# Kernel tuning notes

Measured on AMD Instinct MI355X. Metric: run time of the kernel, lower is better.

The kernel has to match this reference:

```python
import jax, jax.numpy as jnp
import numpy as np

K = 64
M = 256
V = 5000

def setup_inputs() -> dict:
    key = jax.random.key(0)
    ks = jax.random.split(key, 8)
    feat_x = jax.random.normal(ks[0], (1, V, M), dtype=jnp.float32)
    feat_y = jax.random.normal(ks[1], (1, V, M), dtype=jnp.float32)
    evals_x = jnp.sort(jax.random.uniform(ks[2], (1, K), dtype=jnp.float32))
    evals_y = jnp.sort(jax.random.uniform(ks[3], (1, K), dtype=jnp.float32))
    evecs_trans_x = jax.random.normal(ks[4], (1, K, V), dtype=jnp.float32) / np.sqrt(V)
    evecs_trans_y = jax.random.normal(ks[5], (1, K, V), dtype=jnp.float32) / np.sqrt(V)
    eye = jnp.eye(K, dtype=jnp.float32)
    sqrtMk_x = (eye + 0.05 * jax.random.normal(ks[6], (K, K), dtype=jnp.float32))[None]
    sqrtMk_y = (eye + 0.05 * jax.random.normal(ks[7], (K, K), dtype=jnp.float32))[None]
    return {"feat_x": feat_x, "feat_y": feat_y, "evals_x": evals_x, "evals_y": evals_y,
            "evecs_trans_x": evecs_trans_x, "evecs_trans_y": evecs_trans_y,
            "sqrtMk_x": sqrtMk_x, "sqrtMk_y": sqrtMk_y}

LMBDA = 0.001

def _fmap(fx, fy, ex, ey, tx, ty, sx, sy):
    # squeeze batch dim of 1 (as in torch .squeeze())
    fx, fy = fx[0], fy[0]            # [V, m]
    ex, ey = ex[0], ey[0]            # [k]
    tx, ty = tx[0], ty[0]            # [k, V]
    sx, sy = sx[0], sy[0]            # [k, k]
    A = tx @ fx                      # [k, m] spectral coeffs of feat_x
    B = sy @ (ty @ fy)               # adapt_feature=True: premultiply by sqrtMk_y
    k, m = A.shape
    vec_B = B.T.reshape(m * k, 1)
    At_Ik = jnp.kron(A.T, sy)        # [m*k, k*k] (adapt_feature -> Ik = sqrtMk_y)
    first = At_Ik.T @ At_Ik          # [k^2, k^2]
    # adapt_mask=True branch
    inv_sx = jnp.linalg.inv(sx)
    lx = jnp.diag(ex)
    ly = jnp.diag(ey)
    lx_Ik = jnp.kron(lx @ inv_sx, sy)
    Ik_ly = jnp.kron(inv_sx, sy @ ly)
    Delta = lx_Ik - Ik_ly
    second = Delta.T @ Delta
    rhs = At_Ik.T @ vec_B
    op = first + LMBDA * second
    C = jnp.linalg.solve(op, rhs)
    return C.reshape(k, k).T[None]   # [1, k, k]

def reference(feat_x, feat_y, evals_x, evals_y, evecs_trans_x, evecs_trans_y, sqrtMk_x, sqrtMk_y):
    # bidirectional=False -> only Cxy (Cyx is None in the torch module)
    return _fmap(feat_x, feat_y, evals_x, evals_y, evecs_trans_x, evecs_trans_y, sqrtMk_x, sqrtMk_y)
```

## Files before the change

### kernel.cpp

```cpp
#include <hip/hip_runtime.h>

#define LMBDA 0.001f
#define NS_SY 4
#define NS_G  5
#define NS_SX 5
#define OUTER 3
#define LDP 68

#define WS_A    0
#define WS_FY   16384
#define WS_G1   32768
#define WS_T1   36864
#define WS_R2   40960
#define WS_R4   45056
#define WS_GINV 49152
#define WS_C    53248
#define WS_FYAT 57344
#define WS_FLAGS 61440

#define FMA4(ar, xs, b) { ar[0]=fmaf((xs),(b).x,ar[0]); ar[1]=fmaf((xs),(b).y,ar[1]); \
                          ar[2]=fmaf((xs),(b).z,ar[2]); ar[3]=fmaf((xs),(b).w,ar[3]); }

template<int SA, int SB>
__device__ __forceinline__ void mm64(const float* __restrict__ A,
                                     const float* __restrict__ B,
                                     int ti, int tj, float a[4][4]) {
    #pragma unroll 4
    for (int k = 0; k < 64; k += 4) {
        float4 av0 = *(const float4*)&A[(4 * ti + 0) * SA + k];
        float4 av1 = *(const float4*)&A[(4 * ti + 1) * SA + k];
        float4 av2 = *(const float4*)&A[(4 * ti + 2) * SA + k];
        float4 av3 = *(const float4*)&A[(4 * ti + 3) * SA + k];
        float4 b0 = *(const float4*)&B[(k + 0) * SB + 4 * tj];
        float4 b1 = *(const float4*)&B[(k + 1) * SB + 4 * tj];
        float4 b2 = *(const float4*)&B[(k + 2) * SB + 4 * tj];
        float4 b3 = *(const float4*)&B[(k + 3) * SB + 4 * tj];
        FMA4(a[0], av0.x, b0); FMA4(a[0], av0.y, b1); FMA4(a[0], av0.z, b2); FMA4(a[0], av0.w, b3);
        FMA4(a[1], av1.x, b0); FMA4(a[1], av1.y, b1); FMA4(a[1], av1.z, b2); FMA4(a[1], av1.w, b3);
        FMA4(a[2], av2.x, b0); FMA4(a[2], av2.y, b1); FMA4(a[2], av2.z, b2); FMA4(a[2], av2.w, b3);
        FMA4(a[3], av3.x, b0); FMA4(a[3], av3.y, b1); FMA4(a[3], av3.z, b2); FMA4(a[3], av3.w, b3);
    }
}

__device__ __forceinline__ void ns_invert(float* sM, float* sX, float* sY,
                                          int iters, int ti, int tj,
                                          int tid, float alpha)
{
    for (int idx = tid; idx < 4096; idx += 256) {
        int i = idx >> 6, j = idx & 63;
        sX[i * LDP + j] = (i == j) ? alpha : 0.f;
    }
    __syncthreads();
    for (int it = 0; it < iters; ++it) {
        float y[4][4];
        #pragma unroll
        for (int r = 0; r < 4; ++r)
            #pragma unroll
            for (int c = 0; c < 4; ++c) y[r][c] = 0.f;
        mm64<LDP, LDP>(sM, sX, ti, tj, y);
        #pragma unroll
        for (int r = 0; r < 4; ++r) {
            float4 v = {y[r][0], y[r][1], y[r][2], y[r][3]};
            *(float4*)&sY[(4 * ti + r) * 64 + 4 * tj] = v;
        }
        __syncthreads();
        float z[4][4];
        #pragma unroll
        for (int r = 0; r < 4; ++r)
            #pragma unroll
            for (int c = 0; c < 4; ++c) z[r][c] = 0.f;
        mm64<LDP, 64>(sX, sY, ti, tj, z);
        __syncthreads();
        #pragma unroll
        for (int r = 0; r < 4; ++r) {
            float4 xv = *(const float4*)&sX[(4 * ti + r) * LDP + 4 * tj];
            xv.x = 2.f * xv.x - z[r][0];
            xv.y = 2.f * xv.y - z[r][1];
            xv.z = 2.f * xv.z - z[r][2];
            xv.w = 2.f * xv.w - z[r][3];
            *(float4*)&sX[(4 * ti + r) * LDP + 4 * tj] = xv;
        }
        __syncthreads();
    }
}

__device__ __forceinline__ void wait_ge(int* flag, int target, int tid) {
    if (tid == 0) {
        while (__hip_atomic_load(flag, __ATOMIC_ACQUIRE, __HIP_MEMORY_SCOPE_AGENT) < target)
            __builtin_amdgcn_s_sleep(2);
    }
    __syncthreads();
    __threadfence();
}

__device__ __forceinline__ void signal_one(int* flag, int tid) {
    __syncthreads();
    __threadfence();
    if (tid == 0)
        (void)__hip_atomic_fetch_add(flag, 1, __ATOMIC_RELEASE, __HIP_MEMORY_SCOPE_AGENT);
}

__global__ __launch_bounds__(256, 1) void fused_fmnet(
    const float* __restrict__ fx, const float* __restrict__ fy,
    const float* __restrict__ ex, const float* __restrict__ ey,
    const float* __restrict__ tx, const float* __restrict__ ty,
    const float* __restrict__ sx, const float* __restrict__ sy,
    float* __restrict__ ws, float* __restrict__ out)
{
    extern __shared__ __align__(16) float lds[];
    int* flags = (int*)(ws + WS_FLAGS);
    const int tid = threadIdx.x;
    const int ti = tid >> 4, tj = tid & 15;
    const int bid = blockIdx.x;

    if (bid < 216) {
        float* sT = lds;
        float* sF = lds + 4352;
        const int gx = bid & 7, gy = bid >> 3;
        const int mat = gx >> 2;
        const int m0 = (gx & 3) << 6;
        const float* __restrict__ T = mat ? ty : tx;
        const float* __restrict__ F = mat ? fy : fx;
        float* __restrict__ Out = ws + (mat ? WS_FY : WS_A);

        float acc[4][4];
        #pragma unroll
        for (int r = 0; r < 4; ++r)
            #pragma unroll
            for (int c = 0; c < 4; ++c) acc[r][c] = 0.f;

        for (int sc = gy; sc * 64 < 5000; sc += 27) {
            const int v0 = sc << 6;
            int vlen = 5000 - v0; if (vlen > 64) vlen = 64;
            #pragma unroll
            for (int w = 0; w < 4; ++w) {
                const int fidx = tid + (w << 8);
                const int row = fidx >> 4, q = fidx & 15;
                const int vv = q << 2;
                if (vv < vlen) {
                    float4 val = *(const float4*)(T + (size_t)row * 5000 + v0 + vv);
                    sT[(vv + 0) * LDP + row] = val.x;
                    sT[(vv + 1) * LDP + row] = val.y;
                    sT[(vv + 2) * LDP + row] = val.z;
                    sT[(vv + 3) * LDP + row] = val.w;
                }
                if (row < vlen) {
                    *(float4*)&sF[row * LDP + (q << 2)] =
                        *(const float4*)(F + (size_t)(v0 + row) * 256 + m0 + (q << 2));
                }
            }
            __syncthreads();
            for (int v = 0; v < vlen; ++v) {
                float4 av = *(const float4*)&sT[v * LDP + 4 * ti];
                float4 bv = *(const float4*)&sF[v * LDP + 4 * tj];
                FMA4(acc[0], av.x, bv); FMA4(acc[1], av.y, bv);
                FMA4(acc[2], av.z, bv); FMA4(acc[3], av.w, bv);
            }
            __syncthreads();
        }
        #pragma unroll
        for (int r = 0; r < 4; ++r)
            #pragma unroll
            for (int c = 0; c < 4; ++c)
                atomicAdd(&Out[(4 * ti + r) * 256 + m0 + 4 * tj + c], acc[r][c]);
        __syncthreads();
        __threadfence();
        if (tid == 0) {
            (void)__hip_atomic_fetch_add(&flags[gx], 1, __ATOMIC_RELEASE, __HIP_MEMORY_SCOPE_AGENT);
            (void)__hip_atomic_fetch_add(&flags[10], 1, __ATOMIC_RELEASE, __HIP_MEMORY_SCOPE_AGENT);
        }
    } else if (bid < 220) {
        const int ch = bid - 216;
        wait_ge(&flags[ch], 27, tid);
        float* sA = lds;
        for (int idx = tid; idx < 1024; idx += 256) {
            int i = idx >> 4, m4 = (idx & 15) << 2;
            *(float4*)&sA[i * LDP + m4] =
                *(const float4*)&ws[WS_A + i * 256 + (ch << 6) + m4];
        }
        __syncthreads();
        float a[4][4];
        #pragma unroll
        for (int r = 0; r < 4; ++r)
            #pragma unroll
            for (int c = 0; c < 4; ++c) a[r][c] = 0.f;
        for (int m = 0; m < 64; m += 4) {
            float4 av[4], bv[4];
            #pragma unroll
            for (int r = 0; r < 4; ++r) av[r] = *(const float4*)&sA[(4 * ti + r) * LDP + m];
            #pragma unroll
            for (int c = 0; c < 4; ++c) bv[c] = *(const float4*)&sA[(4 * tj + c) * LDP + m];
            #pragma unroll
            for (int r = 0; r < 4; ++r)
                #pragma unroll
                for (int c = 0; c < 4; ++c)
                    a[r][c] += av[r].x * bv[c].x + av[r].y * bv[c].y
                             + av[r].z * bv[c].z + av[r].w * bv[c].w;
        }
        #pragma unroll
        for (int r = 0; r < 4; ++r)
            #pragma unroll
            for (int c = 0; c < 4; ++c)
                atomicAdd(&ws[WS_G1 + (4 * ti + r) * 64 + 4 * tj + c], a[r][c]);
        __syncthreads();
        __threadfence();
        if (tid == 0)
            (void)__hip_atomic_fetch_add(&flags[8], 1, __ATOMIC_RELEASE, __HIP_MEMORY_SCOPE_AGENT);
    } else if (bid == 220) {
        float* sSy = lds;
        float* sXx = lds + 4352;
        float* sYy = lds + 8704;
        float* sH  = lds + 12800;
        float* sV  = lds + 16896;
        for (int idx = tid; idx < 1024; idx += 256) {
            int i = idx >> 4, j4 = (idx & 15) << 2;
            *(float4*)&sSy[i * LDP + j4] = *(const float4*)&sy[i * 64 + j4];
        }
        if (tid < 64) sV[tid] = ey[tid];
        __syncthreads();
        {
            float h[4][4];
            #pragma unroll
            for (int r = 0; r < 4; ++r)
                #pragma unroll
                for (int c = 0; c < 4; ++c) h[r][c] = 0.f;
            for (int k = 0; k < 64; ++k) {
                float4 av = *(const float4*)&sSy[k * LDP + 4 * ti];
                float4 bv = *(const float4*)&sSy[k * LDP + 4 * tj];
                FMA4(h[0], av.x, bv); FMA4(h[1], av.y, bv);
                FMA4(h[2], av.z, bv); FMA4(h[3], av.w, bv);
            }
            #pragma unroll
            for (int r = 0; r < 4; ++r) {
                float4 v = {h[r][0], h[r][1], h[r][2], h[r][3]};
                *(float4*)&sH[(4 * ti + r) * 64 + 4 * tj] = v;
            }
        }
        __syncthreads();
        ns_invert(sSy, sXx, sYy, NS_SY, ti, tj, tid, 1.0f);
        {
            float h[4][4];
            #pragma unroll
            for (int r = 0; r < 4; ++r)
                #pragma unroll
                for (int c = 0; c < 4; ++c) h[r][c] = 0.f;
            for (int m = 0; m < 64; m += 4) {
                float4 av[4], bv[4];
                #pragma unroll
                for (int r = 0; r < 4; ++r) av[r] = *(const float4*)&sXx[(4 * ti + r) * LDP + m];
                #pragma unroll
                for (int c = 0; c < 4; ++c) bv[c] = *(const float4*)&sXx[(4 * tj + c) * LDP + m];
                #pragma unroll
                for (int r = 0; r < 4; ++r)
                    #pragma unroll
                    for (int c = 0; c < 4; ++c)
                        h[r][c] += av[r].x * bv[c].x + av[r].y * bv[c].y
                                 + av[r].z * bv[c].z + av[r].w * bv[c].w;
            }
            __syncthreads();
            #pragma unroll
            for (int r = 0; r < 4; ++r) {
                float4 v = {h[r][0], h[r][1], h[r][2], h[r][3]};
                *(float4*)&sSy[(4 * ti + r) * LDP + 4 * tj] = v;
            }
        }
        __syncthreads();
        {
            float a[4][4];
            #pragma unroll
            for (int r = 0; r < 4; ++r)
                #pragma unroll
                for (int c = 0; c < 4; ++c) a[r][c] = 0.f;
            #pragma unroll 4
            for (int k = 0; k < 64; k += 4) {
                float4 av[4];
                #pragma unroll
                for (int r = 0; r < 4; ++r) av[r] = *(const float4*)&sSy[(4 * ti + r) * LDP + k];
                #pragma unroll
                for (int q = 0; q < 4; ++q) {
                    float e = sV[k + q];
                    float4 bv = *(const float4*)&sH[(k + q) * 64 + 4 * tj];
                    bv.x *= e; bv.y *= e; bv.z *= e; bv.w *= e;
                    float xq[4] = {av[0].x, av[1].x, av[2].x, av[3].x};
                    if (q == 1) { xq[0]=av[0].y; xq[1]=av[1].y; xq[2]=av[2].y; xq[3]=av[3].y; }
                    if (q == 2) { xq[0]=av[0].z; xq[1]=av[1].z; xq[2]=av[2].z; xq[3]=av[3].z; }
                    if (q == 3) { xq[0]=av[0].w; xq[1]=av[1].w; xq[2]=av[2].w; xq[3]=av[3].w; }
                    #pragma unroll
                    for (int r = 0; r < 4; ++r) FMA4(a[r], xq[r], bv);
                }
            }
            #pragma unroll
            for (int r = 0; r < 4; ++r) {
                float4 v = {a[r][0], a[r][1], a[r][2], a[r][3]};
                *(float4*)&ws[WS_C + (4 * ti + r) * 64 + 4 * tj] = v;
            }
        }
        signal_one(&flags[9], tid);
    } else if (bid == 221) {
        float* sM = lds;
        float* sX = lds + 4352;
        float* sY = lds + 8704;
        float* sV = lds + 12800;
        for (int idx = tid; idx < 1024; idx += 256) {
            int i = idx >> 4, j4 = (idx & 15) << 2;
            *(float4*)&sM[i * LDP + j4] = *(const float4*)&sx[i * 64 + j4];
        }
        if (tid < 64) sV[tid] = ex[tid];
        __syncthreads();
        ns_invert(sM, sX, sY, NS_SX, ti, tj, tid, 1.0f);
        float aR2[4][4], aR4[4][4], aT1[4][4];
        #pragma unroll
        for (int r = 0; r < 4; ++r)
            #pragma unroll
            for (int c = 0; c < 4; ++c) { aR2[r][c] = 0.f; aR4[r][c] = 0.f; aT1[r][c] = 0.f; }
        for (int k = 0; k < 64; ++k) {
            float e = sV[k], e2 = e * e;
            float4 av = *(const float4*)&sX[k * LDP + 4 * ti];
            float4 bv = *(const float4*)&sX[k * LDP + 4 * tj];
            float avv[4] = {av.x, av.y, av.z, av.w};
            #pragma unroll
            for (int r = 0; r < 4; ++r) {
                FMA4(aR4[r], avv[r], bv);
                float ea = e * avv[r];
                FMA4(aR2[r], ea, bv);
                float e2a = e2 * avv[r];
                FMA4(aT1[r], e2a, bv);
            }
        }
        #pragma unroll
        for (int r = 0; r < 4; ++r) {
            int o = (4 * ti + r) * 64 + 4 * tj;
            float4 v2 = {aR2[r][0], aR2[r][1], aR2[r][2], aR2[r][3]};
            float4 v4 = {aR4[r][0], aR4[r][1], aR4[r][2], aR4[r][3]};
            float4 v1 = {aT1[r][0], aT1[r][1], aT1[r][2], aT1[r][3]};
            *(float4*)&ws[WS_R2 + o] = v2;
            *(float4*)&ws[WS_R4 + o] = v4;
            *(float4*)&ws[WS_T1 + o] = v1;
        }
        signal_one(&flags[9], tid);
    } else if (bid == 222) {
        wait_ge(&flags[8], 4, tid);
        float* sG = lds;
        float* sX = lds + 4352;
        float* sY = lds + 8704;
        float* sV = lds + 12800;
        for (int idx = tid; idx < 1024; idx += 256) {
            int i = idx >> 4, j4 = (idx & 15) << 2;
            *(float4*)&sG[i * LDP + j4] = *(const float4*)&ws[WS_G1 + i * 64 + j4];
        }
        __syncthreads();
        if (tid < 64) {
            float s = 0.f;
            for (int j4 = 0; j4 < 64; j4 += 4) {
                float4 v = *(const float4*)&sG[tid * LDP + j4];
                s += v.x * v.x + v.y * v.y + v.z * v.z + v.w * v.w;
            }
            sV[tid] = s;
            sV[64 + tid] = sG[tid * LDP + tid];
        }
        __syncthreads();
        float f2 = 0.f, tr = 0.f;
        for (int i = 0; i < 64; ++i) { f2 += sV[i]; tr += sV[64 + i]; }
        ns_invert(sG, sX, sY, NS_G, ti, tj, tid, tr / f2);
        for (int idx = tid; idx < 1024; idx += 256) {
            int i = idx >> 4, j4 = (idx & 15) << 2;
            *(float4*)&ws[WS_GINV + i * 64 + j4] = *(const float4*)&sX[i * LDP + j4];
        }
        signal_one(&flags[9], tid);
    } else if (bid == 223) {
        wait_ge(&flags[10], 216, tid);
        float* sFy = lds;
        float* sAx = lds + 4352;
        float a[4][4];
        #pragma unroll
        for (int r = 0; r < 4; ++r)
            #pragma unroll
            for (int c = 0; c < 4; ++c) a[r][c] = 0.f;
        for (int ch = 0; ch < 4; ++ch) {
            for (int idx = tid; idx < 1024; idx += 256) {
                int i = idx >> 4, m4 = (idx & 15) << 2;
                *(float4*)&sFy[i * LDP + m4] = *(const float4*)&ws[WS_FY + i * 256 + (ch << 6) + m4];
                *(float4*)&sAx[i * LDP + m4] = *(const float4*)&ws[WS_A  + i * 256 + (ch << 6) + m4];
            }
            __syncthreads();
            for (int m = 0; m < 64; m += 4) {
                float4 av[4], bv[4];
                #pragma unroll
                for (int r = 0; r < 4; ++r) av[r] = *(const float4*)&sFy[(4 * ti + r) * LDP + m];
                #pragma unroll
                for (int c = 0; c < 4; ++c) bv[c] = *(const float4*)&sAx[(4 * tj + c) * LDP + m];
                #pragma unroll
                for (int r = 0; r < 4; ++r)
                    #pragma unroll
                    for (int c = 0; c < 4; ++c)
                        a[r][c] += av[r].x * bv[c].x + av[r].y * bv[c].y
                                 + av[r].z * bv[c].z + av[r].w * bv[c].w;
            }
            __syncthreads();
        }
        #pragma unroll
        for (int r = 0; r < 4; ++r) {
            float4 v = {a[r][0], a[r][1], a[r][2], a[r][3]};
            *(float4*)&ws[WS_FYAT + (4 * ti + r) * 64 + 4 * tj] = v;
        }
        signal_one(&flags[9], tid);
    } else {
        wait_ge(&flags[9], 4, tid);
        float* cM1   = lds;
        float* cR2   = lds + 4096;
        float* cR4   = lds + 8192;
        float* cGinv = lds + 12288;
        float* sE    = lds + 16384;
        float* sX    = lds + 20480;
        float* cC    = lds + 24832;
        float* sW    = lds + 29184;

        for (int idx = tid; idx < 1024; idx += 256) {
            int i = idx >> 4, j4 = (idx & 15) << 2;
            int o = i * 64 + j4;
            float4 g = *(const float4*)&ws[WS_G1 + o];
            float4 t = *(const float4*)&ws[WS_T1 + o];
            float4 m = {fmaf(LMBDA, t.x, g.x), fmaf(LMBDA, t.y, g.y),
                        fmaf(LMBDA, t.z, g.z), fmaf(LMBDA, t.w, g.w)};
            *(float4*)&cM1[o]   = m;
            *(float4*)&cR2[o]   = *(const float4*)&ws[WS_R2 + o];
            *(float4*)&cR4[o]   = *(const float4*)&ws[WS_R4 + o];
            *(float4*)&cGinv[o] = *(const float4*)&ws[WS_GINV + o];
            *(float4*)&cC[i * LDP + j4] = *(const float4*)&ws[WS_C + o];
        }
        float4 eyv = *(const float4*)&ey[4 * ti];
        float eyr[4] = {eyv.x, eyv.y, eyv.z, eyv.w};
        float leyr[4];
        #pragma unroll
        for (int r = 0; r < 4; ++r) leyr[r] = LMBDA * eyr[r];

        float fyr[4][4], xreg[4][4];
        #pragma unroll
        for (int r = 0; r < 4; ++r) {
            float4 v = *(const float4*)&ws[WS_FYAT + (4 * ti + r) * 64 + 4 * tj];
            fyr[r][0] = v.x; fyr[r][1] = v.y; fyr[r][2] = v.z; fyr[r][3] = v.w;
            float4 z = {0.f, 0.f, 0.f, 0.f};
            *(float4*)&sX[(4 * ti + r) * LDP + 4 * tj] = z;
            #pragma unroll
            for (int c = 0; c < 4; ++c) xreg[r][c] = 0.f;
        }
        __syncthreads();

        float E1[4][4];
        for (int it = 0; it < OUTER; ++it) {
            {
                float Sm[4][4], S2[4][4], S4[4][4];
                #pragma unroll
                for (int r = 0; r < 4; ++r)
                    #pragma unroll
                    for (int c = 0; c < 4; ++c) { Sm[r][c] = 0.f; S2[r][c] = 0.f; S4[r][c] = 0.f; }
                #pragma unroll 2
                for (int k = 0; k < 64; k += 4) {
                    float4 av[4];
                    #pragma unroll
                    for (int r = 0; r < 4; ++r)
                        av[r] = *(const float4*)&sX[(4 * ti + r) * LDP + k];
                    #pragma unroll
                    for (int q = 0; q < 4; ++q) {
                        float4 mv = *(const float4*)&cM1[(k + q) * 64 + 4 * tj];
                        float4 qv = *(const float4*)&cR2[(k + q) * 64 + 4 * tj];
                        float4 rv = *(const float4*)&cR4[(k + q) * 64 + 4 * tj];
                        float xq[4] = {av[0].x, av[1].x, av[2].x, av[3].x};
                        if (q == 1) { xq[0]=av[0].y; xq[1]=av[1].y; xq[2]=av[2].y; xq[3]=av[3].y; }
                        if (q == 2) { xq[0]=av[0].z; xq[1]=av[1].z; xq[2]=av[2].z; xq[3]=av[3].z; }
                        if (q == 3) { xq[0]=av[0].w; xq[1]=av[1].w; xq[2]=av[2].w; xq[3]=av[3].w; }
                        #pragma unroll
                        for (int r = 0; r < 4; ++r) {
                            FMA4(Sm[r], xq[r], mv);
                            FMA4(S2[r], xq[r], qv);
                            FMA4(S4[r], xq[r], rv);
                        }
                    }
                }
                #pragma unroll
                for (int r = 0; r < 4; ++r) {
                    float4 e2;
                    e2.x = LMBDA * fmaf(eyr[r], S4[r][0], -S2[r][0]);
                    e2.y = LMBDA * fmaf(eyr[r], S4[r][1], -S2[r][1]);
                    e2.z = LMBDA * fmaf(eyr[r], S4[r][2], -S2[r][2]);
                    e2.w = LMBDA * fmaf(eyr[r], S4[r][3], -S2[r][3]);
                    *(float4*)&sE[(4 * ti + r) * 64 + 4 * tj] = e2;
                    #pragma unroll
                    for (int c = 0; c < 4; ++c)
                        E1[r][c] = fmaf(-leyr[r], S2[r][c], Sm[r][c]);
                }
            }
            __syncthreads();
            {
                float Z[4][4];
                #pragma unroll
                for (int r = 0; r < 4; ++r)
                    #pragma unroll
                    for (int c = 0; c < 4; ++c) Z[r][c] = 0.f;
                mm64<LDP, 64>(cC, sE, ti, tj, Z);
                #pragma unroll
                for (int r = 0; r < 4; ++r) {
                    float4 w;
                    w.x = fyr[r][0] - E1[r][0] - Z[r][0];
                    w.y = fyr[r][1] - E1[r][1] - Z[r][1];
                    w.z = fyr[r][2] - E1[r][2] - Z[r][2];
                    w.w = fyr[r][3] - E1[r][3] - Z[r][3];
                    *(float4*)&sW[(4 * ti + r) * LDP + 4 * tj] = w;
                }
            }
            __syncthreads();
            {
                float dX[4][4];
                #pragma unroll
                for (int r = 0; r < 4; ++r)
                    #pragma unroll
                    for (int c = 0; c < 4; ++c) dX[r][c] = 0.f;
                mm64<LDP, 64>(sW, cGinv, ti, tj, dX);
                #pragma unroll
                for (int r = 0; r < 4; ++r) {
                    float4 v;
                    #pragma unroll
                    for (int c = 0; c < 4; ++c) xreg[r][c] += dX[r][c];
                    v.x = xreg[r][0]; v.y = xreg[r][1]; v.z = xreg[r][2]; v.w = xreg[r][3];
                    *(float4*)&sX[(4 * ti + r) * LDP + 4 * tj] = v;
                    if (it == OUTER - 1)
                        *(float4*)&out[(4 * ti + r) * 64 + 4 * tj] = v;
                }
            }
            if (it == OUTER - 1) break;
            __syncthreads();
        }
    }
}

extern "C" void kernel_launch(void* const* d_in, const int* in_sizes, int n_in,
                              void* d_out, int out_size, void* d_ws, size_t ws_size,
                              hipStream_t stream) {
    (void)in_sizes; (void)n_in; (void)out_size; (void)ws_size;
    const float* fx = (const float*)d_in[0];
    const float* fy = (const float*)d_in[1];
    const float* ex = (const float*)d_in[2];
    const float* ey = (const float*)d_in[3];
    const float* tx = (const float*)d_in[4];
    const float* ty = (const float*)d_in[5];
    const float* sx = (const float*)d_in[6];
    const float* sy = (const float*)d_in[7];
    float* ws = (float*)d_ws;
    float* out = (float*)d_out;

    (void)hipFuncSetAttribute((const void*)fused_fmnet,
                              hipFuncAttributeMaxDynamicSharedMemorySize, 134144);

    (void)hipMemsetAsync(d_ws, 0, (WS_G1 + 4096) * sizeof(float), stream);
    (void)hipMemsetAsync((char*)d_ws + WS_FLAGS * sizeof(float), 0, 64, stream);
    fused_fmnet<<<225, 256, 134144, stream>>>(fx, fy, ex, ey, tx, ty, sx, sy, ws, out);
}
```

Measured before the change: 194.7 us.

## Double threads per block to 512 and restructure Gram/inverse stage scheduling

Raises the block size from 256 to 512 threads, so each thread computes a 4x2 output tile instead of 4x4 in every 64x64 matmul. The four separate A^T A Gram blocks are removed; the Gram product and its inverse appear to be computed inside the final solver block instead, and the grid shrinks to 220 blocks. The flag-based dependencies between stages are rewired to match. The aim is more parallelism on the latency-bound serial small-matrix chain, at the cost of extra barrier participants and possibly more serial work in the final block.

```diff
diff --git a/kernel.cpp b/kernel.cpp
--- a/kernel.cpp
+++ b/kernel.cpp
@@ -9,76 +9,83 @@
 
 #define WS_A    0
 #define WS_FY   16384
-#define WS_G1   32768
-#define WS_T1   36864
-#define WS_R2   40960
-#define WS_R4   45056
-#define WS_GINV 49152
-#define WS_C    53248
-#define WS_FYAT 57344
-#define WS_FLAGS 61440
-
-#define FMA4(ar, xs, b) { ar[0]=fmaf((xs),(b).x,ar[0]); ar[1]=fmaf((xs),(b).y,ar[1]); \
-                          ar[2]=fmaf((xs),(b).z,ar[2]); ar[3]=fmaf((xs),(b).w,ar[3]); }
+#define WS_T1   32768
+#define WS_R2   36864
+#define WS_R4   40960
+#define WS_C    45056
+#define WS_FYAT 49152
+#define WS_FLAGS 53248
+
+#define COMP(v,q) ((q)==0?(v).x:((q)==1?(v).y:((q)==2?(v).z:(v).w)))
 
 template<int SA, int SB>
-__device__ __forceinline__ void mm64(const float* __restrict__ A,
-                                     const float* __restrict__ B,
-                                     int ti, int tj, float a[4][4]) {
+__device__ __forceinline__ void mm64r(const float* __restrict__ A,
+                                      const float* __restrict__ B,
+                                      int ti, int tj, float a[4][2]) {
     #pragma unroll 4
     for (int k = 0; k < 64; k += 4) {
-        float4 av0 = *(const float4*)&A[(4 * ti + 0) * SA + k];
-        float4 av1 = *(const float4*)&A[(4 * ti + 1) * SA + k];
-        float4 av2 = *(const float4*)&A[(4 * ti + 2) * SA + k];
-        float4 av3 = *(const float4*)&A[(4 * ti + 3) * SA + k];
-        float4 b0 = *(const float4*)&B[(k + 0) * SB + 4 * tj];
-        float4 b1 = *(const float4*)&B[(k + 1) * SB + 4 * tj];
-        float4 b2 = *(const float4*)&B[(k + 2) * SB + 4 * tj];
-        float4 b3 = *(const float4*)&B[(k + 3) * SB + 4 * tj];
-        FMA4(a[0], av0.x, b0); FMA4(a[0], av0.y, b1); FMA4(a[0], av0.z, b2); FMA4(a[0], av0.w, b3);
-        FMA4(a[1], av1.x, b0); FMA4(a[1], av1.y, b1); FMA4(a[1], av1.z, b2); FMA4(a[1], av1.w, b3);
-        FMA4(a[2], av2.x, b0); FMA4(a[2], av2.y, b1); FMA4(a[2], av2.z, b2); FMA4(a[2], av2.w, b3);
-        FMA4(a[3], av3.x, b0); FMA4(a[3], av3.y, b1); FMA4(a[3], av3.z, b2); FMA4(a[3], av3.w, b3);
-    }
-}
-
-__device__ __forceinline__ void ns_invert(float* sM, float* sX, float* sY,
+        float4 av[4];
+        #pragma unroll
+        for (int r = 0; r < 4; ++r) av[r] = *(const float4*)&A[(4 * ti + r) * SA + k];
+        #pragma unroll
+        for (int q = 0; q < 4; ++q) {
+            float2 bv = *(const float2*)&B[(k + q) * SB + 2 * tj];
+            #pragma unroll
+            for (int r = 0; r < 4; ++r) {
+                float x = COMP(av[r], q);
+                a[r][0] = fmaf(x, bv.x, a[r][0]);
+                a[r][1] = fmaf(x, bv.y, a[r][1]);
+            }
+        }
+    }
+}
+
+template<int SA, int SB>
+__device__ __forceinline__ void mmdot(const float* __restrict__ A,
+                                      const float* __restrict__ B,
+                                      int ti, int tj, float a[4][2]) {
+    #pragma unroll 4
+    for (int m = 0; m < 64; m += 4) {
+        float4 av[4], bv[2];
+        #pragma unroll
+        for (int r = 0; r < 4; ++r) av[r] = *(const float4*)&A[(4 * ti + r) * SA + m];
+        #pragma unroll
+        for (int c = 0; c < 2; ++c) bv[c] = *(const float4*)&B[(2 * tj + c) * SB + m];
+        #pragma unroll
+        for (int r = 0; r < 4; ++r)
+            #pragma unroll
+            for (int c = 0; c < 2; ++c)
+                a[r][c] += av[r].x * bv[c].x + av[r].y * bv[c].y
+                         + av[r].z * bv[c].z + av[r].w * bv[c].w;
+    }
+}
+
+template<int SM>
+__device__ __forceinline__ void ns_invert(const float* sM, float* sX, float* sY,
                                           int iters, int ti, int tj,
                                           int tid, float alpha)
 {
-    for (int idx = tid; idx < 4096; idx += 256) {
+    for (int idx = tid; idx < 4096; idx += 512) {
         int i = idx >> 6, j = idx & 63;
         sX[i * LDP + j] = (i == j) ? alpha : 0.f;
     }
     __syncthreads();
     for (int it = 0; it < iters; ++it) {
-        float y[4][4];
+        float y[4][2] = {};
+        mm64r<SM, LDP>(sM, sX, ti, tj, y);
         #pragma unroll
         for (int r = 0; r < 4; ++r)
-            #pragma unroll
-            for (int c = 0; c < 4; ++c) y[r][c] = 0.f;
-        mm64<LDP, LDP>(sM, sX, ti, tj, y);
+            *(float2*)&sY[(4 * ti + r) * 64 + 2 * tj] = make_float2(y[r][0], y[r][1]);
+        __syncthreads();
+        float z[4][2] = {};
+        mm64r<LDP, 64>(sX, sY, ti, tj, z);
+        __syncthreads();
         #pragma unroll
         for (int r = 0; r < 4; ++r) {
-            float4 v = {y[r][0], y[r][1], y[r][2], y[r][3]};
-            *(float4*)&sY[(4 * ti + r) * 64 + 4 * tj] = v;
-        }
-        __syncthreads();
-        float z[4][4];
-        #pragma unroll
-        for (int r = 0; r < 4; ++r)
-            #pragma unroll
-            for (int c = 0; c < 4; ++c) z[r][c] = 0.f;
-        mm64<LDP, 64>(sX, sY, ti, tj, z);
-        __syncthreads();
-        #pragma unroll
-        for (int r = 0; r < 4; ++r) {
-            float4 xv = *(const float4*)&sX[(4 * ti + r) * LDP + 4 * tj];
+            float2 xv = *(const float2*)&sX[(4 * ti + r) * LDP + 2 * tj];
             xv.x = 2.f * xv.x - z[r][0];
             xv.y = 2.f * xv.y - z[r][1];
-            xv.z = 2.f * xv.z - z[r][2];
-            xv.w = 2.f * xv.w - z[r][3];
-            *(float4*)&sX[(4 * ti + r) * LDP + 4 * tj] = xv;
+            *(float2*)&sX[(4 * ti + r) * LDP + 2 * tj] = xv;
         }
         __syncthreads();
     }
@@ -100,7 +107,7 @@
         (void)__hip_atomic_fetch_add(flag, 1, __ATOMIC_RELEASE, __HIP_MEMORY_SCOPE_AGENT);
 }
 
-__global__ __launch_bounds__(256, 1) void fused_fmnet(
+__global__ __launch_bounds__(512, 2) void fused_fmnet(
     const float* __restrict__ fx, const float* __restrict__ fy,
     const float* __restrict__ ex, const float* __restrict__ ey,
     const float* __restrict__ tx, const float* __restrict__ ty,
@@ -110,7 +117,7 @@
     extern __shared__ __align__(16) float lds[];
     int* flags = (int*)(ws + WS_FLAGS);
     const int tid = threadIdx.x;
-    const int ti = tid >> 4, tj = tid & 15;
+    const int ti = tid >> 5, tj = tid & 31;
     const int bid = blockIdx.x;
 
     if (bid < 216) {
@@ -123,18 +130,13 @@
         const float* __restrict__ F = mat ? fy : fx;
         float* __restrict__ Out = ws + (mat ? WS_FY : WS_A);
 
-        float acc[4][4];
-        #pragma unroll
-        for (int r = 0; r < 4; ++r)
-            #pragma unroll
-            for (int c = 0; c < 4; ++c) acc[r][c] = 0.f;
-
+        float acc[4][2] = {};
         for (int sc = gy; sc * 64 < 5000; sc += 27) {
             const int v0 = sc << 6;
             int vlen = 5000 - v0; if (vlen > 64) vlen = 64;
             #pragma unroll
-            for (int w = 0; w < 4; ++w) {
-                const int fidx = tid + (w << 8);
+            for (int w = 0; w < 2; ++w) {
+                const int fidx = tid + (w << 9);
                 const int row = fidx >> 4, q = fidx & 15;
                 const int vv = q << 2;
                 if (vv < vlen) {
@@ -150,127 +152,65 @@
                 }
             }
             __syncthreads();
+            #pragma unroll 2
             for (int v = 0; v < vlen; ++v) {
                 float4 av = *(const float4*)&sT[v * LDP + 4 * ti];
-                float4 bv = *(const float4*)&sF[v * LDP + 4 * tj];
-                FMA4(acc[0], av.x, bv); FMA4(acc[1], av.y, bv);
-                FMA4(acc[2], av.z, bv); FMA4(acc[3], av.w, bv);
+                float2 bv = *(const float2*)&sF[v * LDP + 2 * tj];
+                acc[0][0] = fmaf(av.x, bv.x, acc[0][0]); acc[0][1] = fmaf(av.x, bv.y, acc[0][1]);
+                acc[1][0] = fmaf(av.y, bv.x, acc[1][0]); acc[1][1] = fmaf(av.y, bv.y, acc[1][1]);
+                acc[2][0] = fmaf(av.z, bv.x, acc[2][0]); acc[2][1] = fmaf(av.z, bv.y, acc[2][1]);
+                acc[3][0] = fmaf(av.w, bv.x, acc[3][0]); acc[3][1] = fmaf(av.w, bv.y, acc[3][1]);
             }
             __syncthreads();
         }
         #pragma unroll
         for (int r = 0; r < 4; ++r)
             #pragma unroll
-            for (int c = 0; c < 4; ++c)
-                atomicAdd(&Out[(4 * ti + r) * 256 + m0 + 4 * tj + c], acc[r][c]);
-        __syncthreads();
-        __threadfence();
-        if (tid == 0) {
-            (void)__hip_atomic_fetch_add(&flags[gx], 1, __ATOMIC_RELEASE, __HIP_MEMORY_SCOPE_AGENT);
-            (void)__hip_atomic_fetch_add(&flags[10], 1, __ATOMIC_RELEASE, __HIP_MEMORY_SCOPE_AGENT);
-        }
-    } else if (bid < 220) {
-        const int ch = bid - 216;
-        wait_ge(&flags[ch], 27, tid);
-        float* sA = lds;
-        for (int idx = tid; idx < 1024; idx += 256) {
-            int i = idx >> 4, m4 = (idx & 15) << 2;
-            *(float4*)&sA[i * LDP + m4] =
-                *(const float4*)&ws[WS_A + i * 256 + (ch << 6) + m4];
-        }
-        __syncthreads();
-        float a[4][4];
-        #pragma unroll
-        for (int r = 0; r < 4; ++r)
-            #pragma unroll
-            for (int c = 0; c < 4; ++c) a[r][c] = 0.f;
-        for (int m = 0; m < 64; m += 4) {
-            float4 av[4], bv[4];
-            #pragma unroll
-            for (int r = 0; r < 4; ++r) av[r] = *(const float4*)&sA[(4 * ti + r) * LDP + m];
-            #pragma unroll
-            for (int c = 0; c < 4; ++c) bv[c] = *(const float4*)&sA[(4 * tj + c) * LDP + m];
-            #pragma unroll
-            for (int r = 0; r < 4; ++r)
-                #pragma unroll
-                for (int c = 0; c < 4; ++c)
-                    a[r][c] += av[r].x * bv[c].x + av[r].y * bv[c].y
-                             + av[r].z * bv[c].z + av[r].w * bv[c].w;
-        }
-        #pragma unroll
-        for (int r = 0; r < 4; ++r)
-            #pragma unroll
-            for (int c = 0; c < 4; ++c)
-                atomicAdd(&ws[WS_G1 + (4 * ti + r) * 64 + 4 * tj + c], a[r][c]);
+            for (int c = 0; c < 2; ++c)
+                atomicAdd(&Out[(4 * ti + r) * 256 + m0 + 2 * tj + c], acc[r][c]);
         __syncthreads();
         __threadfence();
         if (tid == 0)
-            (void)__hip_atomic_fetch_add(&flags[8], 1, __ATOMIC_RELEASE, __HIP_MEMORY_SCOPE_AGENT);
-    } else if (bid == 220) {
+            (void)__hip_atomic_fetch_add(&flags[mat], 1, __ATOMIC_RELEASE, __HIP_MEMORY_SCOPE_AGENT);
+    } else if (bid == 216) {
         float* sSy = lds;
         float* sXx = lds + 4352;
         float* sYy = lds + 8704;
         float* sH  = lds + 12800;
         float* sV  = lds + 16896;
-        for (int idx = tid; idx < 1024; idx += 256) {
+        for (int idx = tid; idx < 1024; idx += 512) {
             int i = idx >> 4, j4 = (idx & 15) << 2;
             *(float4*)&sSy[i * LDP + j4] = *(const float4*)&sy[i * 64 + j4];
         }
         if (tid < 64) sV[tid] = ey[tid];
         __syncthreads();
         {
-            float h[4][4];
-            #pragma unroll
-            for (int r = 0; r < 4; ++r)
-                #pragma unroll
-                for (int c = 0; c < 4; ++c) h[r][c] = 0.f;
+            float h[4][2] = {};
             for (int k = 0; k < 64; ++k) {
                 float4 av = *(const float4*)&sSy[k * LDP + 4 * ti];
-                float4 bv = *(const float4*)&sSy[k * LDP + 4 * tj];
-                FMA4(h[0], av.x, bv); FMA4(h[1], av.y, bv);
-                FMA4(h[2], av.z, bv); FMA4(h[3], av.w, bv);
-            }
-            #pragma unroll
-            for (int r = 0; r < 4; ++r) {
-                float4 v = {h[r][0], h[r][1], h[r][2], h[r][3]};
-                *(float4*)&sH[(4 * ti + r) * 64 + 4 * tj] = v;
-            }
-        }
-        __syncthreads();
-        ns_invert(sSy, sXx, sYy, NS_SY, ti, tj, tid, 1.0f);
+                float2 bv = *(const float2*)&sSy[k * LDP + 2 * tj];
+                h[0][0] = fmaf(av.x, bv.x, h[0][0]); h[0][1] = fmaf(av.x, bv.y, h[0][1]);
+                h[1][0] = fmaf(av.y, bv.x, h[1][0]); h[1][1] = fmaf(av.y, bv.y, h[1][1]);
+                h[2][0] = fmaf(av.z, bv.x, h[2][0]); h[2][1] = fmaf(av.z, bv.y, h[2][1]);
+                h[3][0] = fmaf(av.w, bv.x, h[3][0]); h[3][1] = fmaf(av.w, bv.y, h[3][1]);
+            }
+            #pragma unroll
+            for (int r = 0; r < 4; ++r)
+                *(float2*)&sH[(4 * ti + r) * 64 + 2 * tj] = make_float2(h[r][0], h[r][1]);
+        }
+        __syncthreads();
+        ns_invert<LDP>(sSy, sXx, sYy, NS_SY, ti, tj, tid, 1.0f);
         {
-            float h[4][4];
+            float h[4][2] = {};
+            mmdot<LDP, LDP>(sXx, sXx, ti, tj, h);
+            __syncthreads();
             #pragma unroll
             for (int r = 0; r < 4; ++r)
-                #pragma unroll
-                for (int c = 0; c < 4; ++c) h[r][c] = 0.f;
-            for (int m = 0; m < 64; m += 4) {
-                float4 av[4], bv[4];
-                #pragma unroll
-                for (int r = 0; r < 4; ++r) av[r] = *(const float4*)&sXx[(4 * ti + r) * LDP + m];
-                #pragma unroll
-                for (int c = 0; c < 4; ++c) bv[c] = *(const float4*)&sXx[(4 * tj + c) * LDP + m];
-                #pragma unroll
-                for (int r = 0; r < 4; ++r)
-                    #pragma unroll
-                    for (int c = 0; c < 4; ++c)
-                        h[r][c] += av[r].x * bv[c].x + av[r].y * bv[c].y
-                                 + av[r].z * bv[c].z + av[r].w * bv[c].w;
-            }
-            __syncthreads();
-            #pragma unroll
-            for (int r = 0; r < 4; ++r) {
-                float4 v = {h[r][0], h[r][1], h[r][2], h[r][3]};
-                *(float4*)&sSy[(4 * ti + r) * LDP + 4 * tj] = v;
-            }
+                *(float2*)&sSy[(4 * ti + r) * LDP + 2 * tj] = make_float2(h[r][0], h[r][1]);
         }
         __syncthreads();
         {
-            float a[4][4];
-            #pragma unroll
-            for (int r = 0; r < 4; ++r)
-                #pragma unroll
-                for (int c = 0; c < 4; ++c) a[r][c] = 0.f;
+            float a[4][2] = {};
             #pragma unroll 4
             for (int k = 0; k < 64; k += 4) {
                 float4 av[4];
@@ -279,133 +219,77 @@
                 #pragma unroll
                 for (int q = 0; q < 4; ++q) {
                     float e = sV[k + q];
-                    float4 bv = *(const float4*)&sH[(k + q) * 64 + 4 * tj];
-                    bv.x *= e; bv.y *= e; bv.z *= e; bv.w *= e;
-                    float xq[4] = {av[0].x, av[1].x, av[2].x, av[3].x};
-                    if (q == 1) { xq[0]=av[0].y; xq[1]=av[1].y; xq[2]=av[2].y; xq[3]=av[3].y; }
-                    if (q == 2) { xq[0]=av[0].z; xq[1]=av[1].z; xq[2]=av[2].z; xq[3]=av[3].z; }
-                    if (q == 3) { xq[0]=av[0].w; xq[1]=av[1].w; xq[2]=av[2].w; xq[3]=av[3].w; }
+                    float2 bv = *(const float2*)&sH[(k + q) * 64 + 2 * tj];
+                    bv.x *= e; bv.y *= e;
                     #pragma unroll
-                    for (int r = 0; r < 4; ++r) FMA4(a[r], xq[r], bv);
-                }
-            }
-            #pragma unroll
-            for (int r = 0; r < 4; ++r) {
-                float4 v = {a[r][0], a[r][1], a[r][2], a[r][3]};
-                *(float4*)&ws[WS_C + (4 * ti + r) * 64 + 4 * tj] = v;
-            }
-        }
-        signal_one(&flags[9], tid);
-    } else if (bid == 221) {
+                    for (int r = 0; r < 4; ++r) {
+                        float x = COMP(av[r], q);
+                        a[r][0] = fmaf(x, bv.x, a[r][0]);
+                        a[r][1] = fmaf(x, bv.y, a[r][1]);
+                    }
+                }
+            }
+            #pragma unroll
+            for (int r = 0; r < 4; ++r)
+                *(float2*)&ws[WS_C + (4 * ti + r) * 64 + 2 * tj] = make_float2(a[r][0], a[r][1]);
+        }
+        signal_one(&flags[2], tid);
+    } else if (bid == 217) {
         float* sM = lds;
         float* sX = lds + 4352;
         float* sY = lds + 8704;
         float* sV = lds + 12800;
-        for (int idx = tid; idx < 1024; idx += 256) {
+        for (int idx = tid; idx < 1024; idx += 512) {
             int i = idx >> 4, j4 = (idx & 15) << 2;
             *(float4*)&sM[i * LDP + j4] = *(const float4*)&sx[i * 64 + j4];
         }
         if (tid < 64) sV[tid] = ex[tid];
         __syncthreads();
-        ns_invert(sM, sX, sY, NS_SX, ti, tj, tid, 1.0f);
-        float aR2[4][4], aR4[4][4], aT1[4][4];
-        #pragma unroll
-        for (int r = 0; r < 4; ++r)
-            #pragma unroll
-            for (int c = 0; c < 4; ++c) { aR2[r][c] = 0.f; aR4[r][c] = 0.f; aT1[r][c] = 0.f; }
+        ns_invert<LDP>(sM, sX, sY, NS_SX, ti, tj, tid, 1.0f);
+        float aR2[4][2] = {}, aR4[4][2] = {}, aT1[4][2] = {};
         for (int k = 0; k < 64; ++k) {
             float e = sV[k], e2 = e * e;
             float4 av = *(const float4*)&sX[k * LDP + 4 * ti];
-            float4 bv = *(const float4*)&sX[k * LDP + 4 * tj];
-            float avv[4] = {av.x, av.y, av.z, av.w};
+            float2 bv = *(const float2*)&sX[k * LDP + 2 * tj];
             #pragma unroll
             for (int r = 0; r < 4; ++r) {
-                FMA4(aR4[r], avv[r], bv);
-                float ea = e * avv[r];
-                FMA4(aR2[r], ea, bv);
-                float e2a = e2 * avv[r];
-                FMA4(aT1[r], e2a, bv);
+                float p = COMP(av, r);
+                aR4[r][0] = fmaf(p, bv.x, aR4[r][0]); aR4[r][1] = fmaf(p, bv.y, aR4[r][1]);
+                float ep = e * p;
+                aR2[r][0] = fmaf(ep, bv.x, aR2[r][0]); aR2[r][1] = fmaf(ep, bv.y, aR2[r][1]);
+                float e2p = e2 * p;
+                aT1[r][0] = fmaf(e2p, bv.x, aT1[r][0]); aT1[r][1] = fmaf(e2p, bv.y, aT1[r][1]);
             }
         }
         #pragma unroll
         for (int r = 0; r < 4; ++r) {
-            int o = (4 * ti + r) * 64 + 4 * tj;
-            float4 v2 = {aR2[r][0], aR2[r][1], aR2[r][2], aR2[r][3]};
-            float4 v4 = {aR4[r][0], aR4[r][1], aR4[r][2], aR4[r][3]};
-            float4 v1 = {aT1[r][0], aT1[r][1], aT1[r][2], aT1[r][3]};
-            *(float4*)&ws[WS_R2 + o] = v2;
-            *(float4*)&ws[WS_R4 + o] = v4;
-            *(float4*)&ws[WS_T1 + o] = v1;
-        }
-        signal_one(&flags[9], tid);
-    } else if (bid == 222) {
-        wait_ge(&flags[8], 4, tid);
-        float* sG = lds;
-        float* sX = lds + 4352;
-        float* sY = lds + 8704;
-        float* sV = lds + 12800;
-        for (int idx = tid; idx < 1024; idx += 256) {
-            int i = idx >> 4, j4 = (idx & 15) << 2;
-            *(float4*)&sG[i * LDP + j4] = *(const float4*)&ws[WS_G1 + i * 64 + j4];
-        }
-        __syncthreads();
-        if (tid < 64) {
-            float s = 0.f;
-            for (int j4 = 0; j4 < 64; j4 += 4) {
-                float4 v = *(const float4*)&sG[tid * LDP + j4];
-                s += v.x * v.x + v.y * v.y + v.z * v.z + v.w * v.w;
-            }
-            sV[tid] = s;
-            sV[64 + tid] = sG[tid * LDP + tid];
-        }
-        __syncthreads();
-        float f2 = 0.f, tr = 0.f;
-        for (int i = 0; i < 64; ++i) { f2 += sV[i]; tr += sV[64 + i]; }
-        ns_invert(sG, sX, sY, NS_G, ti, tj, tid, tr / f2);
-        for (int idx = tid; idx < 1024; idx += 256) {
-            int i = idx >> 4, j4 = (idx & 15) << 2;
-            *(float4*)&ws[WS_GINV + i * 64 + j4] = *(const float4*)&sX[i * LDP + j4];
-        }
-        signal_one(&flags[9], tid);
-    } else if (bid == 223) {
-        wait_ge(&flags[10], 216, tid);
+            int o = (4 * ti + r) * 64 + 2 * tj;
+            *(float2*)&ws[WS_R2 + o] = make_float2(aR2[r][0], aR2[r][1]);
+            *(float2*)&ws[WS_R4 + o] = make_float2(aR4[r][0], aR4[r][1]);
+            *(float2*)&ws[WS_T1 + o] = make_float2(aT1[r][0], aT1[r][1]);
+        }
+        signal_one(&flags[2], tid);
+    } else if (bid == 218) {
+        wait_ge(&flags[0], 108, tid);
+        wait_ge(&flags[1], 108, tid);
         float* sFy = lds;
         float* sAx = lds + 4352;
-        float a[4][4];
-        #pragma unroll
-        for (int r = 0; r < 4; ++r)
-            #pragma unroll
-            for (int c = 0; c < 4; ++c) a[r][c] = 0.f;
+        float a[4][2] = {};
         for (int ch = 0; ch < 4; ++ch) {
-            for (int idx = tid; idx < 1024; idx += 256) {
+            for (int idx = tid; idx < 1024; idx += 512) {
                 int i = idx >> 4, m4 = (idx & 15) << 2;
                 *(float4*)&sFy[i * LDP + m4] = *(const float4*)&ws[WS_FY + i * 256 + (ch << 6) + m4];
                 *(float4*)&sAx[i * LDP + m4] = *(const float4*)&ws[WS_A  + i * 256 + (ch << 6) + m4];
             }
             __syncthreads();
-            for (int m = 0; m < 64; m += 4) {
-                float4 av[4], bv[4];
-                #pragma unroll
-                for (int r = 0; r < 4; ++r) av[r] = *(const float4*)&sFy[(4 * ti + r) * LDP + m];
-                #pragma unroll
-                for (int c = 0; c < 4; ++c) bv[c] = *(const float4*)&sAx[(4 * tj + c) * LDP + m];
-                #pragma unroll
-                for (int r = 0; r < 4; ++r)
-                    #pragma unroll
-                    for (int c = 0; c < 4; ++c)
-                        a[r][c] += av[r].x * bv[c].x + av[r].y * bv[c].y
-                                 + av[r].z * bv[c].z + av[r].w * bv[c].w;
-            }
-            __syncthreads();
-        }
-        #pragma unroll
-        for (int r = 0; r < 4; ++r) {
-            float4 v = {a[r][0], a[r][1], a[r][2], a[r][3]};
-            *(float4*)&ws[WS_FYAT + (4 * ti + r) * 64 + 4 * tj] = v;
-        }
-        signal_one(&flags[9], tid);
+            mmdot<LDP, LDP>(sFy, sAx, ti, tj, a);
+            __syncthreads();
+        }
+        #pragma unroll
+        for (int r = 0; r < 4; ++r)
+            *(float2*)&ws[WS_FYAT + (4 * ti + r) * 64 + 2 * tj] = make_float2(a[r][0], a[r][1]);
+        signal_one(&flags[2], tid);
     } else {
-        wait_ge(&flags[9], 4, tid);
         float* cM1   = lds;
         float* cR2   = lds + 4096;
         float* cR4   = lds + 8192;
@@ -415,17 +299,50 @@
         float* cC    = lds + 24832;
         float* sW    = lds + 29184;
 
-        for (int idx = tid; idx < 1024; idx += 256) {
+        wait_ge(&flags[0], 108, tid);
+        float g[4][2] = {};
+        for (int ch = 0; ch < 4; ++ch) {
+            for (int idx = tid; idx < 1024; idx += 512) {
+                int i = idx >> 4, m4 = (idx & 15) << 2;
+                *(float4*)&cC[i * LDP + m4] =
+                    *(const float4*)&ws[WS_A + i * 256 + (ch << 6) + m4];
+            }
+            __syncthreads();
+            mmdot<LDP, LDP>(cC, cC, ti, tj, g);
+            __syncthreads();
+        }
+        #pragma unroll
+        for (int r = 0; r < 4; ++r)
+            *(float2*)&cM1[(4 * ti + r) * 64 + 2 * tj] = make_float2(g[r][0], g[r][1]);
+        __syncthreads();
+        if (tid < 64) {
+            float s = 0.f;
+            for (int j4 = 0; j4 < 64; j4 += 4) {
+                float4 v = *(const float4*)&cM1[tid * 64 + j4];
+                s += v.x * v.x + v.y * v.y + v.z * v.z + v.w * v.w;
+            }
+            sW[tid] = s;
+            sW[64 + tid] = cM1[tid * 64 + tid];
+        }
+        __syncthreads();
+        float f2 = 0.f, tr = 0.f;
+        for (int i = 0; i < 64; ++i) { f2 += sW[i]; tr += sW[64 + i]; }
+        ns_invert<64>(cM1, sX, sE, NS_G, ti, tj, tid, tr / f2);
+        for (int idx = tid; idx < 1024; idx += 512) {
+            int i = idx >> 4, j4 = (idx & 15) << 2;
+            *(float4*)&cGinv[i * 64 + j4] = *(const float4*)&sX[i * LDP + j4];
+        }
+        wait_ge(&flags[2], 3, tid);
+        for (int idx = tid; idx < 1024; idx += 512) {
             int i = idx >> 4, j4 = (idx & 15) << 2;
             int o = i * 64 + j4;
-            float4 g = *(const float4*)&ws[WS_G1 + o];
+            float4 gv = *(const float4*)&cM1[o];
             float4 t = *(const float4*)&ws[WS_T1 + o];
-            float4 m = {fmaf(LMBDA, t.x, g.x), fmaf(LMBDA, t.y, g.y),
-                        fmaf(LMBDA, t.z, g.z), fmaf(LMBDA, t.w, g.w)};
-            *(float4*)&cM1[o]   = m;
-            *(float4*)&cR2[o]   = *(const float4*)&ws[WS_R2 + o];
-            *(float4*)&cR4[o]   = *(const float4*)&ws[WS_R4 + o];
-            *(float4*)&cGinv[o] = *(const float4*)&ws[WS_GINV + o];
+            gv.x = fmaf(LMBDA, t.x, gv.x); gv.y = fmaf(LMBDA, t.y, gv.y);
+            gv.z = fmaf(LMBDA, t.z, gv.z); gv.w = fmaf(LMBDA, t.w, gv.w);
+            *(float4*)&cM1[o] = gv;
+            *(float4*)&cR2[o] = *(const float4*)&ws[WS_R2 + o];
+            *(float4*)&cR4[o] = *(const float4*)&ws[WS_R4 + o];
             *(float4*)&cC[i * LDP + j4] = *(const float4*)&ws[WS_C + o];
         }
         float4 eyv = *(const float4*)&ey[4 * ti];
@@ -434,26 +351,20 @@
         #pragma unroll
         for (int r = 0; r < 4; ++r) leyr[r] = LMBDA * eyr[r];
 
-        float fyr[4][4], xreg[4][4];
+        float fyr[4][2], xreg[4][2];
         #pragma unroll
         for (int r = 0; r < 4; ++r) {
-            float4 v = *(const float4*)&ws[WS_FYAT + (4 * ti + r) * 64 + 4 * tj];
-            fyr[r][0] = v.x; fyr[r][1] = v.y; fyr[r][2] = v.z; fyr[r][3] = v.w;
-            float4 z = {0.f, 0.f, 0.f, 0.f};
-            *(float4*)&sX[(4 * ti + r) * LDP + 4 * tj] = z;
-            #pragma unroll
-            for (int c = 0; c < 4; ++c) xreg[r][c] = 0.f;
-        }
-        __syncthreads();
-
-        float E1[4][4];
+            float2 v = *(const float2*)&ws[WS_FYAT + (4 * ti + r) * 64 + 2 * tj];
+            fyr[r][0] = v.x; fyr[r][1] = v.y;
+            *(float2*)&sX[(4 * ti + r) * LDP + 2 * tj] = make_float2(0.f, 0.f);
+            xreg[r][0] = 0.f; xreg[r][1] = 0.f;
+        }
+        __syncthreads();
+
+        float E1[4][2];
         for (int it = 0; it < OUTER; ++it) {
             {
-                float Sm[4][4], S2[4][4], S4[4][4];
-                #pragma unroll
-                for (int r = 0; r < 4; ++r)
-                    #pragma unroll
-                    for (int c = 0; c < 4; ++c) { Sm[r][c] = 0.f; S2[r][c] = 0.f; S4[r][c] = 0.f; }
+                float Sm[4][2] = {}, S2[4][2] = {}, S4[4][2] = {};
                 #pragma unroll 2
                 for (int k = 0; k < 64; k += 4) {
                     float4 av[4];
@@ -462,69 +373,51 @@
                         av[r] = *(const float4*)&sX[(4 * ti + r) * LDP + k];
                     #pragma unroll
                     for (int q = 0; q < 4; ++q) {
-                        float4 mv = *(const float4*)&cM1[(k + q) * 64 + 4 * tj];
-                        float4 qv = *(const float4*)&cR2[(k + q) * 64 + 4 * tj];
-                        float4 rv = *(const float4*)&cR4[(k + q) * 64 + 4 * tj];
-                        float xq[4] = {av[0].x, av[1].x, av[2].x, av[3].x};
-                        if (q == 1) { xq[0]=av[0].y; xq[1]=av[1].y; xq[2]=av[2].y; xq[3]=av[3].y; }
-                        if (q == 2) { xq[0]=av[0].z; xq[1]=av[1].z; xq[2]=av[2].z; xq[3]=av[3].z; }
-                        if (q == 3) { xq[0]=av[0].w; xq[1]=av[1].w; xq[2]=av[2].w; xq[3]=av[3].w; }
+                        float2 mv = *(const float2*)&cM1[(k + q) * 64 + 2 * tj];
+                        float2 qv = *(const float2*)&cR2[(k + q) * 64 + 2 * tj];
+                        float2 rv = *(const float2*)&cR4[(k + q) * 64 + 2 * tj];
                         #pragma unroll
                         for (int r = 0; r < 4; ++r) {
-                            FMA4(Sm[r], xq[r], mv);
-                            FMA4(S2[r], xq[r], qv);
-                            FMA4(S4[r], xq[r], rv);
+                            float x = COMP(av[r], q);
+                            Sm[r][0] = fmaf(x, mv.x, Sm[r][0]); Sm[r][1] = fmaf(x, mv.y, Sm[r][1]);
+                            S2[r][0] = fmaf(x, qv.x, S2[r][0]); S2[r][1] = fmaf(x, qv.y, S2[r][1]);
+                            S4[r][0] = fmaf(x, rv.x, S4[r][0]); S4[r][1] = fmaf(x, rv.y, S4[r][1]);
                         }
                     }
                 }
                 #pragma unroll
                 for (int r = 0; r < 4; ++r) {
-                    float4 e2;
-                    e2.x = LMBDA * fmaf(eyr[r], S4[r][0], -S2[r][0]);
-                    e2.y = LMBDA * fmaf(eyr[r], S4[r][1], -S2[r][1]);
-                    e2.z = LMBDA * fmaf(eyr[r], S4[r][2], -S2[r][2]);
-                    e2.w = LMBDA * fmaf(eyr[r], S4[r][3], -S2[r][3]);
-                    *(float4*)&sE[(4 * ti + r) * 64 + 4 * tj] = e2;
-                    #pragma unroll
-                    for (int c = 0; c < 4; ++c)
-                        E1[r][c] = fmaf(-leyr[r], S2[r][c], Sm[r][c]);
+                    float2 e2v;
+                    e2v.x = LMBDA * fmaf(eyr[r], S4[r][0], -S2[r][0]);
+                    e2v.y = LMBDA * fmaf(eyr[r], S4[r][1], -S2[r][1]);
+                    *(float2*)&sE[(4 * ti + r) * 64 + 2 * tj] = e2v;
+                    E1[r][0] = fmaf(-leyr[r], S2[r][0], Sm[r][0]);
+                    E1[r][1] = fmaf(-leyr[r], S2[r][1], Sm[r][1]);
                 }
             }
             __syncthreads();
             {
-                float Z[4][4];
-                #pragma unroll
-                for (int r = 0; r < 4; ++r)
-                    #pragma unroll
-                    for (int c = 0; c < 4; ++c) Z[r][c] = 0.f;
-                mm64<LDP, 64>(cC, sE, ti, tj, Z);
+                float Z[4][2] = {};
+                mm64r<LDP, 64>(cC, sE, ti, tj, Z);
                 #pragma unroll
                 for (int r = 0; r < 4; ++r) {
-                    float4 w;
+                    float2 w;
                     w.x = fyr[r][0] - E1[r][0] - Z[r][0];
                     w.y = fyr[r][1] - E1[r][1] - Z[r][1];
-                    w.z = fyr[r][2] - E1[r][2] - Z[r][2];
-                    w.w = fyr[r][3] - E1[r][3] - Z[r][3];
-                    *(float4*)&sW[(4 * ti + r) * LDP + 4 * tj] = w;
+                    *(float2*)&sW[(4 * ti + r) * LDP + 2 * tj] = w;
                 }
             }
             __syncthreads();
             {
-                float dX[4][4];
-                #pragma unroll
-                for (int r = 0; r < 4; ++r)
-                    #pragma unroll
-                    for (int c = 0; c < 4; ++c) dX[r][c] = 0.f;
-                mm64<LDP, 64>(sW, cGinv, ti, tj, dX);
+                float dX[4][2] = {};
+                mm64r<LDP, 64>(sW, cGinv, ti, tj, dX);
                 #pragma unroll
                 for (int r = 0; r < 4; ++r) {
-                    float4 v;
-                    #pragma unroll
-                    for (int c = 0; c < 4; ++c) xreg[r][c] += dX[r][c];
-                    v.x = xreg[r][0]; v.y = xreg[r][1]; v.z = xreg[r][2]; v.w = xreg[r][3];
-                    *(float4*)&sX[(4 * ti + r) * LDP + 4 * tj] = v;
+                    xreg[r][0] += dX[r][0]; xreg[r][1] += dX[r][1];
+                    float2 v = make_float2(xreg[r][0], xreg[r][1]);
+                    *(float2*)&sX[(4 * ti + r) * LDP + 2 * tj] = v;
                     if (it == OUTER - 1)
-                        *(float4*)&out[(4 * ti + r) * 64 + 4 * tj] = v;
+                        *(float2*)&out[(4 * ti + r) * 64 + 2 * tj] = v;
                 }
             }
             if (it == OUTER - 1) break;
@@ -551,7 +444,7 @@
     (void)hipFuncSetAttribute((const void*)fused_fmnet,
                               hipFuncAttributeMaxDynamicSharedMemorySize, 134144);
 
-    (void)hipMemsetAsync(d_ws, 0, (WS_G1 + 4096) * sizeof(float), stream);
-    (void)hipMemsetAsync((char*)d_ws + WS_FLAGS * sizeof(float), 0, 64, stream);
-    fused_fmnet<<<225, 256, 134144, stream>>>(fx, fy, ex, ey, tx, ty, sx, sy, ws, out);
-}
+    (void)hipMemsetAsync(d_ws, 0, 2 * 64 * 256 * sizeof(float), stream);
+    (void)hipMemsetAsync((char*)d_ws + (size_t)WS_FLAGS * sizeof(float), 0, 64, stream);
+    fused_fmnet<<<220, 512, 134144, stream>>>(fx, fy, ex, ey, tx, ty, sx, sy, ws, out);
+}
```

Result: no change. 195.4 us (+0.4%).
